# Kernel optimization log

Hardware: AMD Instinct MI355X
Metric: run time of the kernel (lower is better)

The kernel has to match this reference:

```python
import jax, jax.numpy as jnp
import numpy as np

D_K = 64
D_MODEL = 1024
SEQ = 4096
BATCH = 4


def setup_inputs() -> dict:
    key = jax.random.key(0)
    ks = jax.random.split(key, 7)
    s = 1.0 / np.sqrt(D_MODEL)
    return {
        "x": jax.random.normal(ks[0], (BATCH, SEQ, D_MODEL), dtype=jnp.float32),
        "wq": jax.random.uniform(ks[1], (D_K, D_MODEL), jnp.float32, -s, s),
        "bq": jax.random.uniform(ks[2], (D_K,), jnp.float32, -s, s),
        "wk": jax.random.uniform(ks[3], (D_K, D_MODEL), jnp.float32, -s, s),
        "bk": jax.random.uniform(ks[4], (D_K,), jnp.float32, -s, s),
        "wv": jax.random.uniform(ks[5], (D_K, D_MODEL), jnp.float32, -s, s),
        "bv": jax.random.uniform(ks[6], (D_K,), jnp.float32, -s, s),
    }


def reference(x, wq, bq, wk, bk, wv, bv):
    # q,k,v: [B,T,d_k]
    q = jnp.einsum('btc,dc->btd', x, wq) + bq
    k = jnp.einsum('btc,dc->btd', x, wk) + bk
    v = jnp.einsum('btc,dc->btd', x, wv) + bv
    scale = 1.0 / np.sqrt(D_K).astype(np.float32)
    scores = jnp.einsum('bqd,bkd->bqk', q, k) * scale  # [B,T,T]
    T = x.shape[1]
    causal = jnp.tril(jnp.ones((T, T), dtype=bool))
    scores = jnp.where(causal, scores, -jnp.inf)
    sm = jax.nn.softmax(scores, axis=-1)
    return jnp.einsum('bqk,bkd->bqd', sm, v)
```

## Files before the change

### kernel.cpp

```cpp
#include <hip/hip_runtime.h>

typedef __attribute__((ext_vector_type(8))) short short8;
typedef __attribute__((ext_vector_type(4))) short short4v;
typedef __attribute__((ext_vector_type(4))) float f32x4;

#define D_KV   64
#define SEQ    4096
#define NBATCH 4
#define DMODEL 1024

static __device__ __forceinline__ unsigned short f32_to_bf16(float f) {
  unsigned u = __builtin_bit_cast(unsigned, f);
  u = (u + 0x7FFFu + ((u >> 16) & 1u)) >> 16;
  return (unsigned short)u;
}

__global__ __launch_bounds__(256) void wcvt_kernel(
    const float* __restrict__ wq, const float* __restrict__ wk,
    const float* __restrict__ wv, unsigned short* __restrict__ wfrag) {
  const int fid = blockIdx.x * 256 + threadIdx.x;
  const int nt = fid >> 11, ks = (fid >> 6) & 31, lane = fid & 63;
  const int l16 = lane & 15, lq = lane >> 4;
  const float* w = (nt < 4) ? wq : (nt < 8) ? wk : wv;
  const float* src = w + ((nt & 3) * 16 + l16) * DMODEL + ks * 32 + lq * 8;
  short8 v;
#pragma unroll
  for (int j = 0; j < 8; ++j) v[j] = (short)f32_to_bf16(src[j]);
  *reinterpret_cast<short8*>(wfrag + (long)fid * 8) = v;
}

__global__ __launch_bounds__(256) void qkv_proj_kernel(
    const float* __restrict__ x, const unsigned short* __restrict__ wfrag,
    const float* __restrict__ bq, const float* __restrict__ bk,
    const float* __restrict__ bv,
    unsigned short* __restrict__ Qf, unsigned short* __restrict__ Kf,
    unsigned short* __restrict__ Vf) {
  __shared__ __align__(16) unsigned short lds_x[16 * 1024];
  const int tid = threadIdx.x, lane = tid & 63, wave = tid >> 6;
  const int l16 = lane & 15, lq = lane >> 4;
  const long rowbase = (long)blockIdx.x * 16;

  const int srow = tid >> 4, sq = tid & 15;
  const float* sgptr = x + (rowbase + srow) * DMODEL + sq * 4;
  unsigned char* lx = (unsigned char*)lds_x;
#pragma unroll
  for (int s = 0; s < 16; ++s) {
    const f32x4 xv = *reinterpret_cast<const f32x4*>(sgptr + s * 64);
    short4v xs;
#pragma unroll
    for (int j = 0; j < 4; ++j) xs[j] = (short)f32_to_bf16(xv[j]);
    const int woff = srow * 2048 + ((sq * 8 + s * 128) ^ ((srow & 7) << 4));
    *reinterpret_cast<short4v*>(lx + woff) = xs;
  }
  __syncthreads();

  f32x4 acc[3];
#pragma unroll
  for (int i = 0; i < 3; ++i) acc[i] = (f32x4){0.f, 0.f, 0.f, 0.f};

  const unsigned short* wbase = wfrag + (long)(3 * wave) * 16384 + lane * 8;
  const unsigned char* lrow = lx + l16 * 2048;

#pragma unroll 8
  for (int ks = 0; ks < 32; ++ks) {
    const short8 a = *reinterpret_cast<const short8*>(
        lrow + ((ks * 64 + lq * 16) ^ ((l16 & 7) << 4)));
#pragma unroll
    for (int i = 0; i < 3; ++i) {
      const short8 b = *reinterpret_cast<const short8*>(
          wbase + (long)i * 16384 + ks * 512);
      acc[i] = __builtin_amdgcn_mfma_f32_16x16x32_bf16(a, b, acc[i], 0, 0, 0);
    }
  }

#pragma unroll
  for (int i = 0; i < 3; ++i) {
    const int nt = 3 * wave + i;
    const int mat = nt >> 2;
    const int dcol = ((nt & 3) << 4) | l16;
    const float bias = (mat == 0 ? bq : mat == 1 ? bk : bv)[dcol];
    const int c = dcol >> 5, lqp = (dcol >> 3) & 3, jj = dcol & 7;
#pragma unroll
    for (int r = 0; r < 4; ++r) {
      const long t = rowbase + lq * 4 + r;
      const float sum = acc[i][r] + bias;
      if (mat == 0) {
        Qf[(((t >> 4) * 2 + c) * 64 + lqp * 16 + (t & 15)) * 8 + jj] =
            f32_to_bf16(sum * 0.125f);
      } else if (mat == 1) {
        Kf[((((t >> 6) * 4 + ((t >> 4) & 3)) * 2 + c) * 64 + lqp * 16 +
            (t & 15)) * 8 + jj] = f32_to_bf16(sum);
      } else {
        Vf[((((t >> 6) * 4 + (dcol >> 4)) * 2 + ((t >> 5) & 1)) * 64 +
            ((t >> 3) & 3) * 16 + (dcol & 15)) * 8 + (t & 7)] =
            f32_to_bf16(sum);
      }
    }
  }
}

__global__ __launch_bounds__(256) void attn_kernel(
    const unsigned short* __restrict__ Qf, const unsigned short* __restrict__ Kf,
    const unsigned short* __restrict__ Vf, float* __restrict__ out) {
  __shared__ __align__(16) unsigned short p_lds[4][16][72];
  __shared__ __align__(16) float lds_o[4][16][68];
  __shared__ float lds_ml[4][16][2];
  __shared__ float lds_gl[16];

  const int tid = threadIdx.x;
  const int lane = tid & 63;
  const int wave = tid >> 6;
  const int l16 = lane & 15, lq = lane >> 4;
  const int b = blockIdx.y;
  const int tile = 255 - blockIdx.x;
  const int qbase = tile * 16;
  const long qrow = (long)b * SEQ + qbase;

  short8 qf[2];
#pragma unroll
  for (int c = 0; c < 2; ++c)
    qf[c] = *reinterpret_cast<const short8*>(
        Qf + ((qrow >> 4) * 2 + c) * 512 + lane * 8);

  f32x4 o[4];
#pragma unroll
  for (int dt = 0; dt < 4; ++dt) o[dt] = (f32x4){0.f, 0.f, 0.f, 0.f};
  float m = -INFINITY, ell = 0.f;

  const long ktile0 = (long)b * 64;
  const int nkv = qbase / 64 + 1;
  for (int kt = wave; kt < nkv; kt += 4) {
    const int kvbase = kt * 64;
    const unsigned short* kb = Kf + (ktile0 + kt) * 4096 + lane * 8;
    const unsigned short* vb = Vf + (ktile0 + kt) * 4096 + lane * 8;
    f32x4 s[4];
#pragma unroll
    for (int ct = 0; ct < 4; ++ct) s[ct] = (f32x4){0.f, 0.f, 0.f, 0.f};
#pragma unroll
    for (int ct = 0; ct < 4; ++ct)
#pragma unroll
      for (int c = 0; c < 2; ++c) {
        short8 kf = *reinterpret_cast<const short8*>(kb + (ct * 2 + c) * 512);
        s[ct] = __builtin_amdgcn_mfma_f32_16x16x32_bf16(kf, qf[c], s[ct], 0, 0, 0);
      }
    if (kt == nkv - 1) {
      const int qg = qbase + l16;
#pragma unroll
      for (int ct = 0; ct < 4; ++ct)
#pragma unroll
        for (int r = 0; r < 4; ++r)
          if (kvbase + ct * 16 + lq * 4 + r > qg) s[ct][r] = -INFINITY;
    }
    float mx = -INFINITY;
#pragma unroll
    for (int ct = 0; ct < 4; ++ct)
#pragma unroll
      for (int r = 0; r < 4; ++r) mx = fmaxf(mx, s[ct][r]);
    mx = fmaxf(mx, __shfl_xor(mx, 16, 64));
    mx = fmaxf(mx, __shfl_xor(mx, 32, 64));
    const float nm = fmaxf(m, mx);
    const float alpha = __expf(m - nm);
    float rs = 0.f;
#pragma unroll
    for (int ct = 0; ct < 4; ++ct)
#pragma unroll
      for (int r = 0; r < 4; ++r) {
        const float p = __expf(s[ct][r] - nm);
        s[ct][r] = p;
        rs += p;
      }
    rs += __shfl_xor(rs, 16, 64);
    rs += __shfl_xor(rs, 32, 64);
    ell = ell * alpha + rs;
    m = nm;
#pragma unroll
    for (int dt = 0; dt < 4; ++dt) o[dt] *= alpha;
#pragma unroll
    for (int ct = 0; ct < 4; ++ct)
#pragma unroll
      for (int r = 0; r < 4; ++r)
        p_lds[wave][l16][ct * 16 + lq * 4 + r] = f32_to_bf16(s[ct][r]);
    short8 pf[2];
#pragma unroll
    for (int c = 0; c < 2; ++c)
      pf[c] = *reinterpret_cast<const short8*>(&p_lds[wave][l16][c * 32 + lq * 8]);
#pragma unroll
    for (int dt = 0; dt < 4; ++dt)
#pragma unroll
      for (int c = 0; c < 2; ++c) {
        short8 vf = *reinterpret_cast<const short8*>(vb + (dt * 2 + c) * 512);
        o[dt] = __builtin_amdgcn_mfma_f32_16x16x32_bf16(vf, pf[c], o[dt], 0, 0, 0);
      }
  }

  if (lane < 16) {
    lds_ml[wave][l16][0] = m;
    lds_ml[wave][l16][1] = ell;
  }
  __syncthreads();
  const float m0 = lds_ml[0][l16][0], m1 = lds_ml[1][l16][0];
  const float m2 = lds_ml[2][l16][0], m3 = lds_ml[3][l16][0];
  const float g = fmaxf(fmaxf(m0, m1), fmaxf(m2, m3));
  const float gl = lds_ml[0][l16][1] * __expf(m0 - g) +
                   lds_ml[1][l16][1] * __expf(m1 - g) +
                   lds_ml[2][l16][1] * __expf(m2 - g) +
                   lds_ml[3][l16][1] * __expf(m3 - g);
  const float myscale = __expf(m - g);
  if (wave == 0 && lane < 16) lds_gl[l16] = gl;
#pragma unroll
  for (int dt = 0; dt < 4; ++dt)
#pragma unroll
    for (int r = 0; r < 4; ++r)
      lds_o[wave][l16][dt * 16 + lq * 4 + r] = o[dt][r] * myscale;
  __syncthreads();
#pragma unroll
  for (int j = 0; j < 4; ++j) {
    const int e = tid + 256 * j;
    const int row = e >> 6, col = e & 63;
    const float sum = lds_o[0][row][col] + lds_o[1][row][col] +
                      lds_o[2][row][col] + lds_o[3][row][col];
    out[(qrow + row) * D_KV + col] = sum / lds_gl[row];
  }
}

extern "C" void kernel_launch(void* const* d_in, const int* in_sizes, int n_in,
                              void* d_out, int out_size, void* d_ws, size_t ws_size,
                              hipStream_t stream) {
  const float* x  = (const float*)d_in[0];
  const float* wq = (const float*)d_in[1];
  const float* bq = (const float*)d_in[2];
  const float* wk = (const float*)d_in[3];
  const float* bk = (const float*)d_in[4];
  const float* wv = (const float*)d_in[5];
  const float* bv = (const float*)d_in[6];
  float* out = (float*)d_out;

  unsigned short* ws    = (unsigned short*)d_ws;
  unsigned short* wfrag = ws;
  unsigned short* Qf    = ws + 196608;
  unsigned short* Kf    = Qf + 1048576;
  unsigned short* Vf    = Kf + 1048576;

  wcvt_kernel<<<96, 256, 0, stream>>>(wq, wk, wv, wfrag);
  qkv_proj_kernel<<<1024, 256, 0, stream>>>(x, wfrag, bq, bk, bv, Qf, Kf, Vf);
  dim3 ag(256, NBATCH);
  attn_kernel<<<ag, 256, 0, stream>>>(Qf, Kf, Vf, out);
}
```

Baseline: 68.46 us.

## Restructure QKV projection with LDS-staged weights and pipelined x chunk loads

The projection kernel now has each block handle 32 rows and half of the 12 output n-tiles. The weight fragments for its 6 n-tiles are staged into LDS with global_load_lds in two phases, and x is streamed in 128-column chunks through a 3-buffer ring, with the next chunk's global load issued before computing on the current one. This replaces per-MFMA global weight reads and the up-front load of the whole x tile. It aims to cut redundant global weight traffic and overlap x loads with MFMA work. The cost is about 120KB of LDS per block (one block per CU) and twice as many blocks, each reading x for its n-half, so the global reads of x double.

```diff
diff --git a/kernel.cpp b/kernel.cpp
--- a/kernel.cpp
+++ b/kernel.cpp
@@ -1,7 +1,6 @@
 #include <hip/hip_runtime.h>
 
 typedef __attribute__((ext_vector_type(8))) short short8;
-typedef __attribute__((ext_vector_type(4))) short short4v;
 typedef __attribute__((ext_vector_type(4))) float f32x4;
 
 #define D_KV   64
@@ -13,6 +12,12 @@
   unsigned u = __builtin_bit_cast(unsigned, f);
   u = (u + 0x7FFFu + ((u >> 16) & 1u)) >> 16;
   return (unsigned short)u;
+}
+
+static __device__ __forceinline__ void gload_lds16(const void* gsrc, void* ldst) {
+  __builtin_amdgcn_global_load_lds(
+      (const __attribute__((address_space(1))) void*)gsrc,
+      (__attribute__((address_space(3))) void*)ldst, 16, 0, 0);
 }
 
 __global__ __launch_bounds__(256) void wcvt_kernel(
@@ -29,61 +34,110 @@
   *reinterpret_cast<short8*>(wfrag + (long)fid * 8) = v;
 }
 
-__global__ __launch_bounds__(256) void qkv_proj_kernel(
+__global__ __launch_bounds__(256, 1) void qkv_proj_kernel(
     const float* __restrict__ x, const unsigned short* __restrict__ wfrag,
     const float* __restrict__ bq, const float* __restrict__ bk,
     const float* __restrict__ bv,
     unsigned short* __restrict__ Qf, unsigned short* __restrict__ Kf,
     unsigned short* __restrict__ Vf) {
-  __shared__ __align__(16) unsigned short lds_x[16 * 1024];
+  __shared__ __align__(16) unsigned short wlds[49152];
+  __shared__ __align__(16) unsigned short xlds[12288];
   const int tid = threadIdx.x, lane = tid & 63, wave = tid >> 6;
   const int l16 = lane & 15, lq = lane >> 4;
-  const long rowbase = (long)blockIdx.x * 16;
-
-  const int srow = tid >> 4, sq = tid & 15;
-  const float* sgptr = x + (rowbase + srow) * DMODEL + sq * 4;
-  unsigned char* lx = (unsigned char*)lds_x;
-#pragma unroll
-  for (int s = 0; s < 16; ++s) {
-    const f32x4 xv = *reinterpret_cast<const f32x4*>(sgptr + s * 64);
-    short4v xs;
-#pragma unroll
-    for (int j = 0; j < 4; ++j) xs[j] = (short)f32_to_bf16(xv[j]);
-    const int woff = srow * 2048 + ((sq * 8 + s * 128) ^ ((srow & 7) << 4));
-    *reinterpret_cast<short4v*>(lx + woff) = xs;
-  }
+  const int h = blockIdx.x & 1;
+  const long rowbase = (long)(blockIdx.x >> 1) * 32;
+  const int h6 = h * 6;
+  const int sub = wave >> 1;
+  const int ntl0 = (wave & 1) * 3;
+  unsigned char* wl = (unsigned char*)wlds;
+  unsigned char* xl = (unsigned char*)xlds;
+  const unsigned char* wfb = (const unsigned char*)wfrag;
+
+  const int xr_ = tid >> 3, xcb = (tid & 7) * 32;
+  const float* xrow = x + (rowbase + xr_) * DMODEL;
+  const int xswz = (xr_ & 7) << 4;
+
+  f32x4 acc[3];
+#pragma unroll
+  for (int i = 0; i < 3; ++i) acc[i] = (f32x4){0.f, 0.f, 0.f, 0.f};
+
+  f32x4 xg[4];
+
+#define STAGE_W(ph)                                                           \
+  {                                                                           \
+    _Pragma("unroll")                                                         \
+    for (int i2 = 0; i2 < 24; ++i2) {                                         \
+      const int d = wave * 24576 + i2 * 1024;               \
+      const int ntl = d >> 14, ksl = (d >> 10) & 15;                          \
+      gload_lds16(wfb + (((h6 + ntl) * 32 + (ph) * 16 + ksl) << 10) + lane * 16, \
+                  wl + d);                                                    \
+    }                                                                         \
+  }
+#define XLOAD(c)                                                              \
+  {                                                                           \
+    const float* p = xrow + (c) * 128 + (tid & 7) * 16;                       \
+    xg[0] = *reinterpret_cast<const f32x4*>(p);                               \
+    xg[1] = *reinterpret_cast<const f32x4*>(p + 4);                           \
+    xg[2] = *reinterpret_cast<const f32x4*>(p + 8);                           \
+    xg[3] = *reinterpret_cast<const f32x4*>(p + 12);                          \
+  }
+#define XWRITE(c)                                                             \
+  {                                                                           \
+    short8 s0, s1;                                                            \
+    _Pragma("unroll")                                                         \
+    for (int j = 0; j < 4; ++j) {                                             \
+      s0[j] = (short)f32_to_bf16(xg[0][j]);                                   \
+      s0[4 + j] = (short)f32_to_bf16(xg[1][j]);                               \
+      s1[j] = (short)f32_to_bf16(xg[2][j]);                                   \
+      s1[4 + j] = (short)f32_to_bf16(xg[3][j]);                               \
+    }                                                                         \
+    unsigned char* base = xl + ((c) % 3) * 8192 + xr_ * 256;                  \
+    *reinterpret_cast<short8*>(base + (xcb ^ xswz)) = s0;                     \
+    *reinterpret_cast<short8*>(base + ((xcb + 16) ^ xswz)) = s1;              \
+  }
+
+  STAGE_W(0);
+  XLOAD(0); XWRITE(0);
+  XLOAD(1); XWRITE(1);
   __syncthreads();
 
-  f32x4 acc[3];
-#pragma unroll
-  for (int i = 0; i < 3; ++i) acc[i] = (f32x4){0.f, 0.f, 0.f, 0.f};
-
-  const unsigned short* wbase = wfrag + (long)(3 * wave) * 16384 + lane * 8;
-  const unsigned char* lrow = lx + l16 * 2048;
-
-#pragma unroll 8
-  for (int ks = 0; ks < 32; ++ks) {
-    const short8 a = *reinterpret_cast<const short8*>(
-        lrow + ((ks * 64 + lq * 16) ^ ((l16 & 7) << 4)));
-#pragma unroll
-    for (int i = 0; i < 3; ++i) {
-      const short8 b = *reinterpret_cast<const short8*>(
-          wbase + (long)i * 16384 + ks * 512);
-      acc[i] = __builtin_amdgcn_mfma_f32_16x16x32_bf16(a, b, acc[i], 0, 0, 0);
+  const int arow = sub * 16 + l16;
+  const int aswz = (arow & 7) << 4;
+
+  for (int ck = 0; ck < 8; ++ck) {
+    if (ck < 6) XLOAD(ck + 2);
+    const unsigned char* xbuf = xl + (ck % 3) * 8192 + arow * 256;
+#pragma unroll
+    for (int kc = 0; kc < 4; ++kc) {
+      const short8 a = *reinterpret_cast<const short8*>(
+          xbuf + ((kc * 64 + lq * 16) ^ aswz));
+      const int ksl = (ck & 3) * 4 + kc;
+#pragma unroll
+      for (int i = 0; i < 3; ++i) {
+        const short8 b = *reinterpret_cast<const short8*>(
+            wl + (((ntl0 + i) * 16 + ksl) << 10) + lane * 16);
+        acc[i] = __builtin_amdgcn_mfma_f32_16x16x32_bf16(a, b, acc[i], 0, 0, 0);
+      }
     }
+    __syncthreads();
+    if (ck < 6) XWRITE(ck + 2);
+    if (ck == 3) {
+      STAGE_W(1);
+      __syncthreads();
+    }
   }
 
 #pragma unroll
   for (int i = 0; i < 3; ++i) {
-    const int nt = 3 * wave + i;
+    const int nt = h6 + ntl0 + i;
     const int mat = nt >> 2;
     const int dcol = ((nt & 3) << 4) | l16;
     const float bias = (mat == 0 ? bq : mat == 1 ? bk : bv)[dcol];
     const int c = dcol >> 5, lqp = (dcol >> 3) & 3, jj = dcol & 7;
 #pragma unroll
-    for (int r = 0; r < 4; ++r) {
-      const long t = rowbase + lq * 4 + r;
-      const float sum = acc[i][r] + bias;
+    for (int rr = 0; rr < 4; ++rr) {
+      const long t = rowbase + sub * 16 + lq * 4 + rr;
+      const float sum = acc[i][rr] + bias;
       if (mat == 0) {
         Qf[(((t >> 4) * 2 + c) * 64 + lqp * 16 + (t & 15)) * 8 + jj] =
             f32_to_bf16(sum * 0.125f);
@@ -97,6 +151,9 @@
       }
     }
   }
+#undef STAGE_W
+#undef XLOAD
+#undef XWRITE
 }
 
 __global__ __launch_bounds__(256) void attn_kernel(
```

Result: slower. 86.09 us (+25.8%).

## Split x conversion into separate fragment-layout kernel and batch loads in projection

Applied to the files above, without the earlier changes.

Adds a kernel that converts x to bf16 and writes it out in MFMA fragment order. The projection kernel then reads A fragments straight from global memory with no LDS staging or block barrier, and issues each chunk's A and W loads in batches ahead of its MFMAs. The intent is to drop the LDS round trip and the synchronisation from the projection and raise memory-level parallelism. The cost is an extra kernel launch plus an extra global write and read of the bf16 copy of x, about 32 MB, in exchange for the simpler projection.

```diff
diff --git a/kernel.cpp b/kernel.cpp
--- a/kernel.cpp
+++ b/kernel.cpp
@@ -1,7 +1,6 @@
 #include <hip/hip_runtime.h>
 
 typedef __attribute__((ext_vector_type(8))) short short8;
-typedef __attribute__((ext_vector_type(4))) short short4v;
 typedef __attribute__((ext_vector_type(4))) float f32x4;
 
 #define D_KV   64
@@ -13,6 +12,40 @@
   unsigned u = __builtin_bit_cast(unsigned, f);
   u = (u + 0x7FFFu + ((u >> 16) & 1u)) >> 16;
   return (unsigned short)u;
+}
+
+__global__ __launch_bounds__(256) void xfrag_kernel(
+    const float* __restrict__ x, unsigned short* __restrict__ xfrag) {
+  __shared__ unsigned short lt[16 * 1024];
+  const int tid = threadIdx.x;
+  const long T = blockIdx.x;
+  {
+    const int row = tid >> 4, seg = tid & 15;
+    const float* src = x + (T * 16 + row) * DMODEL + seg * 64;
+    unsigned short* dst = lt + row * 1024 + seg * 64;
+#pragma unroll
+    for (int j = 0; j < 8; ++j) {
+      const f32x4 f0 = *reinterpret_cast<const f32x4*>(src + j * 8);
+      const f32x4 f1 = *reinterpret_cast<const f32x4*>(src + j * 8 + 4);
+      short8 s;
+#pragma unroll
+      for (int q = 0; q < 4; ++q) {
+        s[q] = (short)f32_to_bf16(f0[q]);
+        s[4 + q] = (short)f32_to_bf16(f1[q]);
+      }
+      *reinterpret_cast<short8*>(dst + j * 8) = s;
+    }
+  }
+  __syncthreads();
+  unsigned short* dst = xfrag + T * 16384;
+#pragma unroll
+  for (int i = 0; i < 8; ++i) {
+    const int slot = i * 256 + tid;
+    const int lane2 = slot & 63, ks = slot >> 6;
+    const short8 v = *reinterpret_cast<const short8*>(
+        lt + (lane2 & 15) * 1024 + ks * 32 + (lane2 >> 4) * 8);
+    *reinterpret_cast<short8*>(dst + slot * 8) = v;
+  }
 }
 
 __global__ __launch_bounds__(256) void wcvt_kernel(
@@ -29,48 +62,40 @@
   *reinterpret_cast<short8*>(wfrag + (long)fid * 8) = v;
 }
 
-__global__ __launch_bounds__(256) void qkv_proj_kernel(
-    const float* __restrict__ x, const unsigned short* __restrict__ wfrag,
+__global__ __launch_bounds__(256, 2) void qkv_proj_kernel(
+    const unsigned short* __restrict__ xfrag,
+    const unsigned short* __restrict__ wfrag,
     const float* __restrict__ bq, const float* __restrict__ bk,
     const float* __restrict__ bv,
     unsigned short* __restrict__ Qf, unsigned short* __restrict__ Kf,
     unsigned short* __restrict__ Vf) {
-  __shared__ __align__(16) unsigned short lds_x[16 * 1024];
   const int tid = threadIdx.x, lane = tid & 63, wave = tid >> 6;
   const int l16 = lane & 15, lq = lane >> 4;
-  const long rowbase = (long)blockIdx.x * 16;
-
-  const int srow = tid >> 4, sq = tid & 15;
-  const float* sgptr = x + (rowbase + srow) * DMODEL + sq * 4;
-  unsigned char* lx = (unsigned char*)lds_x;
-#pragma unroll
-  for (int s = 0; s < 16; ++s) {
-    const f32x4 xv = *reinterpret_cast<const f32x4*>(sgptr + s * 64);
-    short4v xs;
-#pragma unroll
-    for (int j = 0; j < 4; ++j) xs[j] = (short)f32_to_bf16(xv[j]);
-    const int woff = srow * 2048 + ((sq * 8 + s * 128) ^ ((srow & 7) << 4));
-    *reinterpret_cast<short4v*>(lx + woff) = xs;
-  }
-  __syncthreads();
+  const long T = blockIdx.x;
+
+  const unsigned short* abase = xfrag + T * 16384 + lane * 8;
+  const unsigned short* wbase = wfrag + (long)(3 * wave) * 16384 + lane * 8;
 
   f32x4 acc[3];
 #pragma unroll
   for (int i = 0; i < 3; ++i) acc[i] = (f32x4){0.f, 0.f, 0.f, 0.f};
 
-  const unsigned short* wbase = wfrag + (long)(3 * wave) * 16384 + lane * 8;
-  const unsigned char* lrow = lx + l16 * 2048;
-
-#pragma unroll 8
-  for (int ks = 0; ks < 32; ++ks) {
-    const short8 a = *reinterpret_cast<const short8*>(
-        lrow + ((ks * 64 + lq * 16) ^ ((l16 & 7) << 4)));
-#pragma unroll
-    for (int i = 0; i < 3; ++i) {
-      const short8 b = *reinterpret_cast<const short8*>(
-          wbase + (long)i * 16384 + ks * 512);
-      acc[i] = __builtin_amdgcn_mfma_f32_16x16x32_bf16(a, b, acc[i], 0, 0, 0);
-    }
+#pragma unroll
+  for (int ck = 0; ck < 8; ++ck) {
+    short8 a[4], bw[12];
+#pragma unroll
+    for (int kc = 0; kc < 4; ++kc)
+      a[kc] = *reinterpret_cast<const short8*>(abase + (ck * 4 + kc) * 512);
+#pragma unroll
+    for (int j = 0; j < 12; ++j)
+      bw[j] = *reinterpret_cast<const short8*>(
+          wbase + (long)(j >> 2) * 16384 + (ck * 4 + (j & 3)) * 512);
+#pragma unroll
+    for (int kc = 0; kc < 4; ++kc)
+#pragma unroll
+      for (int i = 0; i < 3; ++i)
+        acc[i] = __builtin_amdgcn_mfma_f32_16x16x32_bf16(
+            a[kc], bw[i * 4 + kc], acc[i], 0, 0, 0);
   }
 
 #pragma unroll
@@ -81,9 +106,9 @@
     const float bias = (mat == 0 ? bq : mat == 1 ? bk : bv)[dcol];
     const int c = dcol >> 5, lqp = (dcol >> 3) & 3, jj = dcol & 7;
 #pragma unroll
-    for (int r = 0; r < 4; ++r) {
-      const long t = rowbase + lq * 4 + r;
-      const float sum = acc[i][r] + bias;
+    for (int rr = 0; rr < 4; ++rr) {
+      const long t = T * 16 + lq * 4 + rr;
+      const float sum = acc[i][rr] + bias;
       if (mat == 0) {
         Qf[(((t >> 4) * 2 + c) * 64 + lqp * 16 + (t & 15)) * 8 + jj] =
             f32_to_bf16(sum * 0.125f);
@@ -240,9 +265,11 @@
   unsigned short* Qf    = ws + 196608;
   unsigned short* Kf    = Qf + 1048576;
   unsigned short* Vf    = Kf + 1048576;
-
+  unsigned short* xfrag = Vf + 1048576;
+
+  xfrag_kernel<<<1024, 256, 0, stream>>>(x, xfrag);
   wcvt_kernel<<<96, 256, 0, stream>>>(wq, wk, wv, wfrag);
-  qkv_proj_kernel<<<1024, 256, 0, stream>>>(x, wfrag, bq, bk, bv, Qf, Kf, Vf);
+  qkv_proj_kernel<<<1024, 256, 0, stream>>>(xfrag, wfrag, bq, bk, bv, Qf, Kf, Vf);
   dim3 ag(256, NBATCH);
   attn_kernel<<<ag, 256, 0, stream>>>(Qf, Kf, Vf, out);
 }
```

After: 75.45 us. +10.2%, slower.
